# Performance work log

Hardware: AMD Instinct MI355X
Metric: run time of the kernel (lower is better)

Reference implementation:

```python
import jax, jax.numpy as jnp
import numpy as np

N = 100_000          # nodes
E = 3_200_000        # edges (avg degree 32)
NEG_SLOPE = 0.2      # PyG GATConv default


def _gat_conv(x, src, dst, W, a_src, a_dst, b, n):
    """Single-head PyG-style GATConv. src/dst already include self-loops."""
    h = x @ W                                   # [N, F_out]
    logits = (h @ a_src)[src] + (h @ a_dst)[dst]  # [E']
    e = jax.nn.leaky_relu(logits, NEG_SLOPE)
    m = jax.ops.segment_max(e, dst, num_segments=n)
    ex = jnp.exp(e - m[dst])                    # stable ragged softmax over in-edges
    s = jax.ops.segment_sum(ex, dst, num_segments=n)
    alpha = ex / (s[dst] + 1e-16)
    out = jax.ops.segment_sum(h[src] * alpha[:, None], dst, num_segments=n)
    return out + b


def setup_inputs() -> dict:
    key = jax.random.key(0)
    ks = jax.random.split(key, 20)
    x = jax.random.normal(ks[0], (N, 3), dtype=jnp.float32)
    edge_index = jax.random.randint(ks[1], (2, E), 0, N, dtype=jnp.int64)

    def lin(k, fin, fout):
        return jax.random.normal(k, (fin, fout), dtype=jnp.float32) * (1.0 / np.sqrt(fin))

    def att(k, f):
        return jax.random.normal(k, (f,), dtype=jnp.float32) * (1.0 / np.sqrt(f))

    inp = {"x": x, "edge_index": edge_index}
    # forward-direction convs
    inp["W1"], inp["as1"], inp["ad1"], inp["b1"] = lin(ks[2], 3, 16), att(ks[3], 16), att(ks[4], 16), jnp.zeros((16,), jnp.float32)
    inp["W2"], inp["as2"], inp["ad2"], inp["b2"] = lin(ks[5], 16, 1), att(ks[6], 1), att(ks[7], 1), jnp.zeros((1,), jnp.float32)
    # reverse-direction convs
    inp["W1r"], inp["as1r"], inp["ad1r"], inp["b1r"] = lin(ks[8], 3, 16), att(ks[9], 16), att(ks[10], 16), jnp.zeros((16,), jnp.float32)
    inp["W2r"], inp["as2r"], inp["ad2r"], inp["b2r"] = lin(ks[11], 16, 1), att(ks[12], 1), att(ks[13], 1), jnp.zeros((1,), jnp.float32)
    return inp


def reference(x, edge_index, W1, as1, ad1, b1, W2, as2, ad2, b2,
              W1r, as1r, ad1r, b1r, W2r, as2r, ad2r, b2r):
    n = x.shape[0]
    loops = jnp.arange(n, dtype=edge_index.dtype)
    # forward direction (self-loops appended, as PyG add_self_loops=True)
    src = jnp.concatenate([edge_index[0], loops])
    dst = jnp.concatenate([edge_index[1], loops])
    # reverse direction: stack([ei[1], ei[0]]) then self-loops
    rsrc = jnp.concatenate([edge_index[1], loops])
    rdst = jnp.concatenate([edge_index[0], loops])

    xf = jax.nn.relu(_gat_conv(x, src, dst, W1, as1, ad1, b1, n))
    xf = _gat_conv(xf, src, dst, W2, as2, ad2, b2, n)

    xr = jax.nn.relu(_gat_conv(x, rsrc, rdst, W1r, as1r, ad1r, b1r, n))
    xr = _gat_conv(xr, rsrc, rdst, W2r, as2r, ad2r, b2r, n)

    return (xf + xr) * 0.5
```

## Files before the change

### kernel.cpp

```cpp
#include <hip/hip_runtime.h>
#include <math.h>

#define NSLOPE 0.2f
#define BSH 8
#define BNODES 256
#define NID_MASK 0x1FFFF
#define SENT 0xFFFFFFFFu
#define CAP 10240
#define GB 512
#define RE 2048
#define SLOT 12
#define SPILLCAP 256
#define CPT (CAP / 512)

__device__ __forceinline__ float lrelu(float v) { return v > 0.f ? v : NSLOPE * v; }

__global__ void k_flag(const unsigned long long* __restrict__ p, int* __restrict__ flag) {
    int t = threadIdx.x;
    bool bad = false;
#pragma unroll
    for (int i = 0; i < 4; i++)
        if (p[t * 4 + i] >= (1ull << 32)) bad = true;
    unsigned long long mask = __ballot(bad);
    if (t == 0) *flag = (mask == 0ull) ? 1 : 0;
}

__global__ void k_prep(const float* __restrict__ x,
                       const float* __restrict__ as1, const float* __restrict__ ad1,
                       const float* __restrict__ as1r, const float* __restrict__ ad1r,
                       const float* __restrict__ W1, const float* __restrict__ W1r,
                       float4* __restrict__ rec4f, float4* __restrict__ rec4r,
                       float* __restrict__ s1df, float* __restrict__ s1dr,
                       int* __restrict__ gcur, int NS, int N) {
    int i = blockIdx.x * blockDim.x + threadIdx.x;
    if (i < NS) gcur[i] = 0;
    if (i >= N) return;
    float x0 = x[3 * i], x1 = x[3 * i + 1], x2 = x[3 * i + 2];
    float ssf = 0.f, sdf = 0.f, ssr = 0.f, sdr = 0.f;
#pragma unroll
    for (int k = 0; k < 16; k++) {
        float hf = x0 * W1[k] + x1 * W1[16 + k] + x2 * W1[32 + k];
        ssf += hf * as1[k];
        sdf += hf * ad1[k];
        float hr = x0 * W1r[k] + x1 * W1r[16 + k] + x2 * W1r[32 + k];
        ssr += hr * as1r[k];
        sdr += hr * ad1r[k];
    }
    rec4f[i] = make_float4(x0, x1, x2, ssf);
    rec4r[i] = make_float4(x0, x1, x2, ssr);
    s1df[i] = sdf; s1dr[i] = sdr;
}

__global__ void __launch_bounds__(512) k_scatsort(
        const void* __restrict__ ei, long long E, const int* __restrict__ flag,
        int NB, int NS, int* __restrict__ gcur, unsigned* __restrict__ bin) {
    extern __shared__ unsigned smem[];
    unsigned* slots = smem;
    int* cnt  = (int*)(slots + (size_t)NS * SLOT);
    int* gpos = cnt + NS;
    int* spill_s = gpos + NS;
    int* spill_p = spill_s + SPILLCAP;
    unsigned* spill_r = (unsigned*)(spill_p + SPILLCAP);
    int* spn = (int*)(spill_r + SPILLCAP);

    int t = threadIdx.x;
    int fl = *flag;
    long long chunk = (E + GB - 1) / GB;
    long long cstart = (long long)blockIdx.x * chunk;
    long long cend = cstart + chunk; if (cend > E) cend = E;

    for (long long rs = cstart; rs < cend; rs += RE) {
        int ne = (int)min((long long)RE, cend - rs);
        for (int c = t; c < NS; c += 512) cnt[c] = 0;
        if (t == 0) *spn = 0;
        __syncthreads();
#pragma unroll
        for (int k = 0; k < RE / 512; k++) {
            int idx = t + k * 512;
            if (idx < ne) {
                long long i = rs + idx;
                int u, v;
                if (fl) { const long long* p = (const long long*)ei; u = (int)p[i]; v = (int)p[E + i]; }
                else    { const int* p = (const int*)ei; u = p[i]; v = p[E + i]; }
                unsigned r0 = (unsigned)u | ((unsigned)(v & (BNODES - 1)) << 17);
                int s0 = v >> BSH;
                unsigned r1 = (unsigned)v | ((unsigned)(u & (BNODES - 1)) << 17);
                int s1 = NB + (u >> BSH);
                int p0 = atomicAdd(&cnt[s0], 1);
                if (p0 < SLOT) slots[s0 * SLOT + p0] = r0;
                else { int sp = atomicAdd(spn, 1); if (sp < SPILLCAP) { spill_s[sp] = s0; spill_p[sp] = p0; spill_r[sp] = r0; } }
                int p1 = atomicAdd(&cnt[s1], 1);
                if (p1 < SLOT) slots[s1 * SLOT + p1] = r1;
                else { int sp = atomicAdd(spn, 1); if (sp < SPILLCAP) { spill_s[sp] = s1; spill_p[sp] = p1; spill_r[sp] = r1; } }
            }
        }
        __syncthreads();
        for (int c = t; c < NS; c += 512) {
            int n = cnt[c];
            gpos[c] = n ? atomicAdd(&gcur[c], n) : 0;
        }
        __syncthreads();
        for (int c = t; c < NS; c += 512) {
            int n = cnt[c]; if (n > SLOT) n = SLOT;
            int g = gpos[c];
            long long b = (long long)c * CAP;
            for (int j = 0; j < n; j++) {
                int off = g + j;
                if (off < CAP) bin[b + off] = slots[c * SLOT + j];
            }
        }
        int nsp = *spn; if (nsp > SPILLCAP) nsp = SPILLCAP;
        for (int i = t; i < nsp; i += 512) {
            int s = spill_s[i];
            int off = gpos[s] + spill_p[i];
            if (off < CAP) bin[(long long)s * CAP + off] = spill_r[i];
        }
        __syncthreads();
    }
}

__global__ void __launch_bounds__(512) k_bagg1(
        unsigned* __restrict__ bin, const int* __restrict__ gcur,
        const float4* __restrict__ rec4f, const float* __restrict__ s1df,
        const float4* __restrict__ rec4r, const float* __restrict__ s1dr,
        const float* __restrict__ b1, const float* __restrict__ W1,
        const float* __restrict__ W2,
        const float* __restrict__ as2, const float* __restrict__ ad2,
        const float* __restrict__ b1r, const float* __restrict__ W1r,
        const float* __restrict__ W2r,
        const float* __restrict__ as2r, const float* __restrict__ ad2r,
        float2* __restrict__ p2f, float* __restrict__ s2df,
        float2* __restrict__ p2r, float* __restrict__ s2dr,
        int* __restrict__ aoff, int* __restrict__ aend, int NB, int N) {
    int bb = blockIdx.x, dir = blockIdx.y;
    const float4* rec4 = dir ? rec4r : rec4f;
    const float* s1d = dir ? s1dr : s1df;
    const float* b1_ = dir ? b1r : b1;
    const float* W1_ = dir ? W1r : W1;
    const float* W2_ = dir ? W2r : W2;
    float as2v = dir ? as2r[0] : as2[0];
    float ad2v = dir ? ad2r[0] : ad2[0];
    float2* p2 = dir ? p2r : p2f;
    float* s2d = dir ? s2dr : s2df;

    int c = dir * NB + bb;
    long long base = (long long)c * CAP;
    int n = gcur[c]; if (n > CAP) n = CAP;
    int v0 = bb << BSH;
    int nv = N - v0; if (nv > BNODES) nv = BNODES;

    __shared__ int cnt[BNODES];
    __shared__ int loff[BNODES];
    __shared__ unsigned lds_u[CAP];
    int t = threadIdx.x;

    unsigned recs[CPT];
#pragma unroll
    for (int k = 0; k < CPT; k++) {
        int i = t + k * 512;
        recs[k] = (i < n) ? __builtin_nontemporal_load(bin + base + i) : SENT;
    }
    if (t < BNODES) cnt[t] = 0;
    __syncthreads();
#pragma unroll
    for (int k = 0; k < CPT; k++)
        if (recs[k] != SENT) atomicAdd(&cnt[recs[k] >> 17], 1);
    __syncthreads();
    if (t < BNODES) loff[t] = cnt[t];
    __syncthreads();
    for (int od = 1; od < BNODES; od <<= 1) {
        int tmp = (t < BNODES && t >= od) ? loff[t - od] : 0;
        __syncthreads();
        if (t < BNODES) loff[t] += tmp;
        __syncthreads();
    }
    if (t < BNODES) {
        int ex = loff[t] - cnt[t];
        loff[t] = ex;
        cnt[t] = ex;
    }
    __syncthreads();
#pragma unroll
    for (int k = 0; k < CPT; k++)
        if (recs[k] != SENT) {
            int p = atomicAdd(&cnt[recs[k] >> 17], 1);
            lds_u[p] = recs[k] & NID_MASK;
        }
    __syncthreads();
    int node = t >> 1, lane = t & 1;
    float sdv = (node < nv) ? s1d[v0 + node] : 0.f;
    float d = 0.f, a0 = 0.f, a1 = 0.f, a2 = 0.f;
    if (node < nv) {
        int ls = loff[node], le = cnt[node];
        for (int pos = ls + lane; pos < le; pos += 2) {
            unsigned u = lds_u[pos];
            float4 r = rec4[u];
            float w = __expf(lrelu(r.w + sdv));
            d += w; a0 += w * r.x; a1 += w * r.y; a2 += w * r.z;
        }
    }
    d  += __shfl_xor(d, 1);
    a0 += __shfl_xor(a0, 1);
    a1 += __shfl_xor(a1, 1);
    a2 += __shfl_xor(a2, 1);
    if (lane == 0 && node < nv) {
        int v = v0 + node;
        float4 r = rec4[v];
        float w = __expf(lrelu(r.w + sdv));
        float dd = d + w;
        float inv = 1.f / (dd + 1e-16f);
        float m0 = (a0 + w * r.x) * inv;
        float m1 = (a1 + w * r.y) * inv;
        float m2 = (a2 + w * r.z) * inv;
        float h2v = 0.f;
#pragma unroll
        for (int k = 0; k < 16; k++) {
            float o = m0 * W1_[k] + m1 * W1_[16 + k] + m2 * W1_[32 + k] + b1_[k];
            o = fmaxf(o, 0.f);
            h2v += o * W2_[k];
        }
        p2[v] = make_float2(h2v, h2v * as2v);
        s2d[v] = h2v * ad2v;
    }
    for (int i = t; i < n; i += 512) bin[base + i] = lds_u[i];
    if (t < nv) {
        aoff[dir * N + v0 + t] = (int)(base + loff[t]);
        aend[dir * N + v0 + t] = (int)(base + cnt[t]);
    }
}

__global__ void k_agg2(const unsigned* __restrict__ bin,
                       const int* __restrict__ aoff, const int* __restrict__ aend,
                       const float2* __restrict__ p2f, const float* __restrict__ s2df,
                       const float2* __restrict__ p2r, const float* __restrict__ s2dr,
                       const float* __restrict__ b2, const float* __restrict__ b2r,
                       float* __restrict__ out, int N) {
    int tid = blockIdx.x * blockDim.x + threadIdx.x;
    int v = tid >> 3;
    int lane = tid & 7;
    if (v >= N) return;
    float res[2];
#pragma unroll
    for (int dir = 0; dir < 2; dir++) {
        const float2* p2 = dir ? p2r : p2f;
        const float* s2d = dir ? s2dr : s2df;
        float bias = dir ? b2r[0] : b2[0];
        float sd = s2d[v];
        int st = aoff[dir * N + v], en = aend[dir * N + v];
        float d = 0.f, a = 0.f;
        if (lane == 0) {
            float2 ts = p2[v];
            float w = __expf(lrelu(ts.y + sd));
            d = w; a = w * ts.x;
        }
        int j = st + lane;
        for (; j + 24 < en; j += 32) {
            unsigned u0 = __builtin_nontemporal_load(bin + j);
            unsigned u1 = __builtin_nontemporal_load(bin + j + 8);
            unsigned u2 = __builtin_nontemporal_load(bin + j + 16);
            unsigned u3 = __builtin_nontemporal_load(bin + j + 24);
            float2 t0 = p2[u0];
            float2 t1 = p2[u1];
            float2 t2 = p2[u2];
            float2 t3 = p2[u3];
            float w0 = __expf(lrelu(t0.y + sd));
            float w1 = __expf(lrelu(t1.y + sd));
            float w2 = __expf(lrelu(t2.y + sd));
            float w3 = __expf(lrelu(t3.y + sd));
            d += (w0 + w1) + (w2 + w3);
            a += w0 * t0.x + w1 * t1.x + w2 * t2.x + w3 * t3.x;
        }
        for (; j < en; j += 8) {
            unsigned u = __builtin_nontemporal_load(bin + j);
            float2 t = p2[u];
            float w = __expf(lrelu(t.y + sd));
            d += w;
            a += w * t.x;
        }
#pragma unroll
        for (int mask = 1; mask < 8; mask <<= 1) {
            d += __shfl_xor(d, mask);
            a += __shfl_xor(a, mask);
        }
        res[dir] = a / (d + 1e-16f) + bias;
    }
    if (lane == 0) out[v] = 0.5f * (res[0] + res[1]);
}

extern "C" void kernel_launch(void* const* d_in, const int* in_sizes, int n_in,
                              void* d_out, int out_size, void* d_ws, size_t ws_size,
                              hipStream_t stream) {
    const float* x   = (const float*)d_in[0];
    const void*  ei  = d_in[1];
    const float* W1  = (const float*)d_in[2];
    const float* as1 = (const float*)d_in[3];
    const float* ad1 = (const float*)d_in[4];
    const float* b1  = (const float*)d_in[5];
    const float* W2  = (const float*)d_in[6];
    const float* as2 = (const float*)d_in[7];
    const float* ad2 = (const float*)d_in[8];
    const float* b2  = (const float*)d_in[9];
    const float* W1r  = (const float*)d_in[10];
    const float* as1r = (const float*)d_in[11];
    const float* ad1r = (const float*)d_in[12];
    const float* b1r  = (const float*)d_in[13];
    const float* W2r  = (const float*)d_in[14];
    const float* as2r = (const float*)d_in[15];
    const float* ad2r = (const float*)d_in[16];
    const float* b2r  = (const float*)d_in[17];

    const int N = in_sizes[0] / 3;
    const long long E = in_sizes[1] / 2;
    const int NB = (N + BNODES - 1) >> BSH;
    const int NS = 2 * NB;

    char* w = (char*)d_ws;
    size_t o = 0;
    auto A = [&](size_t bytes) { o = (o + 255) & ~(size_t)255; size_t r = o; o += bytes; return r; };
    size_t oFlag = A(64);
    size_t oR4f  = A(sizeof(float4) * N);
    size_t oR4r  = A(sizeof(float4) * N);
    size_t oS1df = A(sizeof(float) * N);
    size_t oS1dr = A(sizeof(float) * N);
    size_t oP2f  = A(sizeof(float2) * N);
    size_t oS2df = A(sizeof(float) * N);
    size_t oP2r  = A(sizeof(float2) * N);
    size_t oS2dr = A(sizeof(float) * N);
    size_t oAoff = A(sizeof(int) * 2 * N);
    size_t oAend = A(sizeof(int) * 2 * N);
    size_t oGcur = A(sizeof(int) * NS);
    size_t oBin  = A(sizeof(unsigned) * (size_t)NS * CAP);
    (void)ws_size; (void)n_in; (void)out_size;

    int*    flag = (int*)(w + oFlag);
    float4* rec4f = (float4*)(w + oR4f);
    float4* rec4r = (float4*)(w + oR4r);
    float*  s1df = (float*)(w + oS1df);
    float*  s1dr = (float*)(w + oS1dr);
    float2* p2f  = (float2*)(w + oP2f);
    float*  s2df = (float*)(w + oS2df);
    float2* p2r  = (float2*)(w + oP2r);
    float*  s2dr = (float*)(w + oS2dr);
    int*    aoff = (int*)(w + oAoff);
    int*    aend = (int*)(w + oAend);
    int*    gcur = (int*)(w + oGcur);
    unsigned* bin = (unsigned*)(w + oBin);

    dim3 gN((N + 255) / 256);
    dim3 gAgg1(NB, 2);
    dim3 gAgg2((N * 8 + 255) / 256);

    size_t smem = sizeof(unsigned) * (size_t)NS * SLOT
                + sizeof(int) * (size_t)NS * 2
                + sizeof(int) * SPILLCAP * 2
                + sizeof(unsigned) * SPILLCAP
                + 64;

    k_flag<<<1, 64, 0, stream>>>((const unsigned long long*)ei, flag);
    k_prep<<<gN, 256, 0, stream>>>(x, as1, ad1, as1r, ad1r, W1, W1r,
                                   rec4f, rec4r, s1df, s1dr, gcur, NS, N);
    k_scatsort<<<GB, 512, smem, stream>>>(ei, E, flag, NB, NS, gcur, bin);
    k_bagg1<<<gAgg1, 512, 0, stream>>>(bin, gcur, rec4f, s1df, rec4r, s1dr,
                                       b1, W1, W2, as2, ad2,
                                       b1r, W1r, W2r, as2r, ad2r,
                                       p2f, s2df, p2r, s2dr, aoff, aend, NB, N);
    k_agg2<<<gAgg2, 256, 0, stream>>>(bin, aoff, aend, p2f, s2df, p2r, s2dr,
                                      b2, b2r, (float*)d_out, N);
}
```

Measured before the change: 257.6 us.

## Widen bucket aggregation to 1024 threads, wave-scan offsets, paired bin writes

The bucket aggregation kernel now runs 1024 threads per block with four lanes per destination node instead of two. Its 256-entry block scan is replaced by a wavefront shuffle scan plus a small cross-wave fixup, which removes most block barriers. The scatter-sort rounds each bucket's reservation up to an even count so slot contents can be written as 8-byte pairs, padding with sentinel entries that later stages skip. This adds sentinel padding and wasted bin capacity in exchange for wider stores, more parallelism per node, and fewer barriers.

Result: faster. 250.8 us (-2.6%).

```diff
diff --git a/kernel.cpp b/kernel.cpp
--- a/kernel.cpp
+++ b/kernel.cpp
@@ -11,7 +11,8 @@
 #define RE 2048
 #define SLOT 12
 #define SPILLCAP 256
-#define CPT (CAP / 512)
+#define BAGT 1024
+#define CPT (CAP / BAGT)
 
 __device__ __forceinline__ float lrelu(float v) { return v > 0.f ? v : NSLOPE * v; }
 
@@ -97,16 +98,27 @@
         __syncthreads();
         for (int c = t; c < NS; c += 512) {
             int n = cnt[c];
-            gpos[c] = n ? atomicAdd(&gcur[c], n) : 0;
+            int rn = (n + 1) & ~1;
+            gpos[c] = rn ? atomicAdd(&gcur[c], rn) : 0;
         }
         __syncthreads();
         for (int c = t; c < NS; c += 512) {
-            int n = cnt[c]; if (n > SLOT) n = SLOT;
+            int n = cnt[c];
+            if (!n) continue;
+            int rn = (n + 1) & ~1;
             int g = gpos[c];
             long long b = (long long)c * CAP;
-            for (int j = 0; j < n; j++) {
-                int off = g + j;
-                if (off < CAP) bin[b + off] = slots[c * SLOT + j];
+            int m = n < SLOT ? n : SLOT;
+            if (g + rn <= CAP) {
+                uint2* bp = (uint2*)(bin + b + g);
+                int np = (m + 1) >> 1;
+                for (int j = 0; j < np; j++) {
+                    unsigned v0 = slots[c * SLOT + 2 * j];
+                    unsigned v1 = (2 * j + 1 < m) ? slots[c * SLOT + 2 * j + 1] : SENT;
+                    bp[j] = make_uint2(v0, v1);
+                }
+                if (n > SLOT && rn > n)
+                    bin[b + g + n] = SENT;
             }
         }
         int nsp = *spn; if (nsp > SPILLCAP) nsp = SPILLCAP;
@@ -119,7 +131,7 @@
     }
 }
 
-__global__ void __launch_bounds__(512) k_bagg1(
+__global__ void __launch_bounds__(BAGT) k_bagg1(
         unsigned* __restrict__ bin, const int* __restrict__ gcur,
         const float4* __restrict__ rec4f, const float* __restrict__ s1df,
         const float4* __restrict__ rec4r, const float* __restrict__ s1dr,
@@ -151,13 +163,14 @@
 
     __shared__ int cnt[BNODES];
     __shared__ int loff[BNODES];
+    __shared__ int segtot[4];
     __shared__ unsigned lds_u[CAP];
     int t = threadIdx.x;
 
     unsigned recs[CPT];
 #pragma unroll
     for (int k = 0; k < CPT; k++) {
-        int i = t + k * 512;
+        int i = t + k * BAGT;
         recs[k] = (i < n) ? __builtin_nontemporal_load(bin + base + i) : SENT;
     }
     if (t < BNODES) cnt[t] = 0;
@@ -166,16 +179,25 @@
     for (int k = 0; k < CPT; k++)
         if (recs[k] != SENT) atomicAdd(&cnt[recs[k] >> 17], 1);
     __syncthreads();
-    if (t < BNODES) loff[t] = cnt[t];
-    __syncthreads();
-    for (int od = 1; od < BNODES; od <<= 1) {
-        int tmp = (t < BNODES && t >= od) ? loff[t - od] : 0;
-        __syncthreads();
-        if (t < BNODES) loff[t] += tmp;
-        __syncthreads();
-    }
     if (t < BNODES) {
-        int ex = loff[t] - cnt[t];
+        int lane = t & 63, w = t >> 6;
+        int val = cnt[t];
+        int incl = val;
+#pragma unroll
+        for (int od = 1; od < 64; od <<= 1) {
+            int up = __shfl_up(incl, od);
+            if (lane >= od) incl += up;
+        }
+        if (lane == 63) segtot[w] = incl;
+        loff[t] = incl - val;
+    }
+    __syncthreads();
+    if (t < BNODES) {
+        int w = t >> 6;
+        int offs = 0;
+#pragma unroll
+        for (int j = 0; j < 4; j++) offs += (j < w) ? segtot[j] : 0;
+        int ex = loff[t] + offs;
         loff[t] = ex;
         cnt[t] = ex;
     }
@@ -187,22 +209,25 @@
             lds_u[p] = recs[k] & NID_MASK;
         }
     __syncthreads();
-    int node = t >> 1, lane = t & 1;
+    int node = t >> 2, lane = t & 3;
     float sdv = (node < nv) ? s1d[v0 + node] : 0.f;
     float d = 0.f, a0 = 0.f, a1 = 0.f, a2 = 0.f;
     if (node < nv) {
         int ls = loff[node], le = cnt[node];
-        for (int pos = ls + lane; pos < le; pos += 2) {
+        for (int pos = ls + lane; pos < le; pos += 4) {
             unsigned u = lds_u[pos];
             float4 r = rec4[u];
             float w = __expf(lrelu(r.w + sdv));
             d += w; a0 += w * r.x; a1 += w * r.y; a2 += w * r.z;
         }
     }
-    d  += __shfl_xor(d, 1);
-    a0 += __shfl_xor(a0, 1);
-    a1 += __shfl_xor(a1, 1);
-    a2 += __shfl_xor(a2, 1);
+#pragma unroll
+    for (int mask = 1; mask < 4; mask <<= 1) {
+        d  += __shfl_xor(d, mask);
+        a0 += __shfl_xor(a0, mask);
+        a1 += __shfl_xor(a1, mask);
+        a2 += __shfl_xor(a2, mask);
+    }
     if (lane == 0 && node < nv) {
         int v = v0 + node;
         float4 r = rec4[v];
@@ -222,7 +247,8 @@
         p2[v] = make_float2(h2v, h2v * as2v);
         s2d[v] = h2v * ad2v;
     }
-    for (int i = t; i < n; i += 512) bin[base + i] = lds_u[i];
+    int nreal = (nv > 0) ? cnt[nv - 1] : 0;
+    for (int i = t; i < nreal; i += BAGT) bin[base + i] = lds_u[i];
     if (t < nv) {
         aoff[dir * N + v0 + t] = (int)(base + loff[t]);
         aend[dir * N + v0 + t] = (int)(base + cnt[t]);
@@ -360,10 +386,10 @@
     k_prep<<<gN, 256, 0, stream>>>(x, as1, ad1, as1r, ad1r, W1, W1r,
                                    rec4f, rec4r, s1df, s1dr, gcur, NS, N);
     k_scatsort<<<GB, 512, smem, stream>>>(ei, E, flag, NB, NS, gcur, bin);
-    k_bagg1<<<gAgg1, 512, 0, stream>>>(bin, gcur, rec4f, s1df, rec4r, s1dr,
-                                       b1, W1, W2, as2, ad2,
-                                       b1r, W1r, W2r, as2r, ad2r,
-                                       p2f, s2df, p2r, s2dr, aoff, aend, NB, N);
+    k_bagg1<<<gAgg1, BAGT, 0, stream>>>(bin, gcur, rec4f, s1df, rec4r, s1dr,
+                                        b1, W1, W2, as2, ad2,
+                                        b1r, W1r, W2r, as2r, ad2r,
+                                        p2f, s2df, p2r, s2dr, aoff, aend, NB, N);
     k_agg2<<<gAgg2, 256, 0, stream>>>(bin, aoff, aend, p2f, s2df, p2r, s2dr,
                                       b2, b2r, (float*)d_out, N);
 }
```
